# Kernel optimization log

Hardware: AMD Instinct MI355X
Metric: run time of the kernel (lower is better)

Reference implementation:

```python
import jax, jax.numpy as jnp
import numpy as np

DEPTH = 18                      # perfect binary tree depth -> N = 2**DEPTH - 1 nodes
N_NODES = 2 ** DEPTH - 1        # 262143
VOCAB, E, H = 2048, 64, 64


def setup_inputs() -> dict:
    key = jax.random.key(0)
    ks = jax.random.split(key, 10)
    token_ids = jax.random.randint(ks[0], (N_NODES,), 0, VOCAB, dtype=jnp.int32)
    emb = jax.random.normal(ks[1], (VOCAB, E), dtype=jnp.float32)
    emb = emb.at[0].set(0.0)  # padding_idx=0 row is zero in torch
    s = 0.1  # keep gates out of hard saturation
    return {
        "token_ids": token_ids,
        "emb": emb,
        "W_iou": jax.random.normal(ks[2], (3 * H, E), dtype=jnp.float32) * s,
        "b_Wiou": jnp.zeros((3 * H,), dtype=jnp.float32),
        "U_iou": jax.random.normal(ks[3], (3 * H, 2 * H), dtype=jnp.float32) * s,
        "b_Uiou": jnp.zeros((3 * H,), dtype=jnp.float32),
        "W_f": jax.random.normal(ks[4], (2 * H, E), dtype=jnp.float32) * s,
        "b_Wf": jnp.zeros((2 * H,), dtype=jnp.float32),
        "U_f": jax.random.normal(ks[5], (2 * H, 2 * H), dtype=jnp.float32) * s,
        "b_Uf": jnp.zeros((2 * H,), dtype=jnp.float32),
        "depth": DEPTH,
    }


def _tree_lstm(token_ids, emb, W_iou, b_Wiou, U_iou, b_Uiou, W_f, b_Wf, U_f, b_Uf, depth):
    """Level-synchronous bottom-up Binary TreeLSTM over a perfect binary tree.

    Node i has children 2i+1 (left), 2i+2 (right); level l occupies
    indices [2**l - 1, 2**(l+1) - 2]. Children of level-l node k sit at
    offsets 2k, 2k+1 of level l+1, so a reshape gives (left, right) pairs.
    """
    Hd = W_f.shape[0] // 2
    h = c = None
    for l in range(depth - 1, -1, -1):
        start, n = 2 ** l - 1, 2 ** l
        x = emb[token_ids[start:start + n]]                    # [n, E]
        if h is None:  # leaves: zero left/right states (both children zero)
            h_cat = jnp.zeros((n, 2 * Hd), dtype=x.dtype)
            c_lr = jnp.zeros((n, 2, Hd), dtype=x.dtype)
        else:
            h_cat = h.reshape(n, 2 * Hd)                        # [h_l | h_r]
            c_lr = c.reshape(n, 2, Hd)
        iou = jax.nn.sigmoid(x @ W_iou.T + b_Wiou + h_cat @ U_iou.T + b_Uiou)
        i_g, o_g, u_g = jnp.split(iou, 3, axis=1)
        u_g = jnp.tanh(u_g)  # faithful: tanh(sigmoid(u_pre)) as in the source
        f = jax.nn.sigmoid(x @ W_f.T + b_Wf + h_cat @ U_f.T + b_Uf)
        f_l, f_r = f[:, :Hd], f[:, Hd:]
        c = i_g * u_g + f_l * c_lr[:, 0] + f_r * c_lr[:, 1]
        h = o_g * jnp.tanh(c)
    return jnp.stack([h, c])  # [2, 1, H]: root (h, c)


def reference(token_ids, emb, W_iou, b_Wiou, U_iou, b_Uiou, W_f, b_Wf, U_f, b_Uf, depth):
    return _tree_lstm(token_ids, emb, W_iou, b_Wiou, U_iou, b_Uiou,
                      W_f, b_Wf, U_f, b_Uf, depth)
```

## Files before the change

kernel.cpp:

```cpp
#include <hip/hip_runtime.h>

typedef __bf16 bf16;
typedef __bf16 bf16x8 __attribute__((ext_vector_type(8)));
typedef float f32x4 __attribute__((ext_vector_type(4)));

#define DEPTH   18
#define N_NODES ((1 << DEPTH) - 1)
#define KDIM    192
#define RDIM    320
#define A_PAD   200
#define LOG2E   1.4426950408889634f

__device__ __forceinline__ float rcpf(float x) { return __builtin_amdgcn_rcpf(x); }
__device__ __forceinline__ float sig2(float p)  { return rcpf(1.f + exp2f(-p)); }
__device__ __forceinline__ float tanhf_(float x){ return 2.f * rcpf(1.f + exp2f(-2.f * LOG2E * x)) - 1.f; }

__device__ __forceinline__ void gates(const f32x4* acc,
        const float4& bI, const float4& bO, const float4& bU,
        const float4& bL, const float4& bR,
        const float4& cl, const float4& cr, float4& c4, float4& h4) {
    const float* pbI = &bI.x; const float* pbO = &bO.x; const float* pbU = &bU.x;
    const float* pbL = &bL.x; const float* pbR = &bR.x;
    const float* pcl = &cl.x; const float* pcr = &cr.x;
    float* pc4 = &c4.x; float* ph4 = &h4.x;
#pragma unroll
    for (int r = 0; r < 4; r++) {
        float i_g = sig2(acc[0][r] + pbI[r]);
        float o_g = sig2(acc[1][r] + pbO[r]);
        float u_g = tanhf_(sig2(acc[2][r] + pbU[r]));
        float fl  = sig2(acc[3][r] + pbL[r]);
        float fr  = sig2(acc[4][r] + pbR[r]);
        float c = i_g * u_g + fl * pcl[r] + fr * pcr[r];
        pc4[r] = c;
        ph4[r] = o_g * tanhf_(c);
    }
}

__global__ void prep_all(const float* __restrict__ emb,
                     const float* __restrict__ W_iou, const float* __restrict__ U_iou,
                     const float* __restrict__ W_f,   const float* __restrict__ U_f,
                     const float* __restrict__ b_Wiou, const float* __restrict__ b_Uiou,
                     const float* __restrict__ b_Wf,   const float* __restrict__ b_Uf,
                     bf16* __restrict__ Wcat, float* __restrict__ bias, bf16* __restrict__ emb16,
                     bf16* __restrict__ leafH, float* __restrict__ leafC) {
    __shared__ __align__(16) bf16 Wl[192 * 72];
    __shared__ __align__(16) bf16 Al[64 * 72];
    const int blk = blockIdx.x, tid = threadIdx.x;
    if (blk < 512) {
        int t = blk * 256 + tid;
        emb16[t] = (bf16)emb[t];
        if (t < RDIM * KDIM) {
            int r = t / KDIM, k = t % KDIM;
            float v;
            if (r < 192) v = (k < 64) ? W_iou[r * 64 + k] : U_iou[r * 128 + (k - 64)];
            else { int rr = r - 192; v = (k < 64) ? W_f[rr * 64 + k] : U_f[rr * 128 + (k - 64)]; }
            Wcat[t] = (bf16)(v * LOG2E);
        }
        if (t < RDIM)
            bias[t] = ((t < 192) ? (b_Wiou[t] + b_Uiou[t]) : (b_Wf[t - 192] + b_Uf[t - 192])) * LOG2E;
        return;
    }
    const int v0 = (blk - 512) * 64;
    for (int i = tid; i < 192 * 64; i += 256) {
        int r = i >> 6, k = i & 63;
        Wl[r * 72 + k] = (bf16)(W_iou[i] * LOG2E);
    }
    for (int i = tid; i < 64 * 64; i += 256) {
        int r = i >> 6, k = i & 63;
        Al[r * 72 + k] = (bf16)emb[(v0 << 6) + i];
    }
    __syncthreads();
    const int wave = tid >> 6, lane = tid & 63;
    const int l15 = lane & 15, quad = lane >> 4;
    const int jw = (wave & 3) * 16, jb = jw + quad * 4;

    f32x4 acc[4][3];
#pragma unroll
    for (int t = 0; t < 4; t++)
#pragma unroll
        for (int g = 0; g < 3; g++) acc[t][g] = (f32x4){0.f, 0.f, 0.f, 0.f};
#pragma unroll
    for (int kb = 0; kb < 2; kb++) {
        bf16x8 wfrag[3], nfrag[4];
#pragma unroll
        for (int g = 0; g < 3; g++)
            wfrag[g] = *(const bf16x8*)(&Wl[(g * 64 + jw + l15) * 72 + kb * 32 + quad * 8]);
#pragma unroll
        for (int t = 0; t < 4; t++)
            nfrag[t] = *(const bf16x8*)(&Al[(t * 16 + l15) * 72 + kb * 32 + quad * 8]);
#pragma unroll
        for (int t = 0; t < 4; t++)
#pragma unroll
            for (int g = 0; g < 3; g++)
                acc[t][g] = __builtin_amdgcn_mfma_f32_16x16x32_bf16(wfrag[g], nfrag[t], acc[t][g], 0, 0, 0);
    }
    float4 bW, bU_;
    bW = *(const float4*)(b_Wiou + jb);       bU_ = *(const float4*)(b_Uiou + jb);
    float4 bI = make_float4((bW.x + bU_.x) * LOG2E, (bW.y + bU_.y) * LOG2E, (bW.z + bU_.z) * LOG2E, (bW.w + bU_.w) * LOG2E);
    bW = *(const float4*)(b_Wiou + 64 + jb);  bU_ = *(const float4*)(b_Uiou + 64 + jb);
    float4 bO = make_float4((bW.x + bU_.x) * LOG2E, (bW.y + bU_.y) * LOG2E, (bW.z + bU_.z) * LOG2E, (bW.w + bU_.w) * LOG2E);
    bW = *(const float4*)(b_Wiou + 128 + jb); bU_ = *(const float4*)(b_Uiou + 128 + jb);
    float4 bU = make_float4((bW.x + bU_.x) * LOG2E, (bW.y + bU_.y) * LOG2E, (bW.z + bU_.z) * LOG2E, (bW.w + bU_.w) * LOG2E);
    const float* pbI = &bI.x; const float* pbO = &bO.x; const float* pbU = &bU.x;
#pragma unroll
    for (int t = 0; t < 4; t++) {
        int v = v0 + t * 16 + l15;
        float4 c4; float* pc4 = &c4.x;
        union { bf16 h[4]; uint2 u; } hp;
#pragma unroll
        for (int r = 0; r < 4; r++) {
            float i_g = sig2(acc[t][0][r] + pbI[r]);
            float o_g = sig2(acc[t][1][r] + pbO[r]);
            float u_g = tanhf_(sig2(acc[t][2][r] + pbU[r]));
            float c = i_g * u_g;
            pc4[r] = c;
            hp.h[r] = (bf16)(o_g * tanhf_(c));
        }
        *(float4*)(leafC + (size_t)v * 64 + jb) = c4;
        *(uint2*)(leafH + (size_t)v * 64 + jb) = hp.u;
    }
}

__global__ __launch_bounds__(256) void pair_pass(
        const bf16* __restrict__ Wcat, const float* __restrict__ bias,
        const bf16* __restrict__ emb16, const int* __restrict__ token_ids,
        const bf16* __restrict__ leafH, const float* __restrict__ leafC,
        bf16* __restrict__ H, float* __restrict__ c_buf) {
    __shared__ __align__(16) bf16 A1[64 * A_PAD];
    __shared__ __align__(16) bf16 A2[32 * A_PAD];
    float* Cc = (float*)A1;
    const int tid = threadIdx.x;
    const int c0 = blockIdx.x * 64;
    const int p0 = c0 >> 1;
    const int sc = 65535, sp = 32767;

    for (int ch = tid; ch < 64 * 8; ch += 256) {
        int row = ch >> 3, k8 = (ch & 7) << 3;
        int tok = token_ids[sc + c0 + row];
        *(uint4*)&A1[row * A_PAD + k8] = *(const uint4*)(emb16 + tok * 64 + k8);
    }
    for (int ch = tid; ch < 64 * 16; ch += 256) {
        int row = ch >> 4, half = (ch >> 3) & 1, k8 = (ch & 7) << 3;
        int gnc = sc + c0 + row;
        int tok = token_ids[2 * gnc + 1 + half];
        *(uint4*)&A1[row * A_PAD + 64 + half * 64 + k8] = *(const uint4*)(leafH + (size_t)tok * 64 + k8);
    }
    for (int ch = tid; ch < 32 * 8; ch += 256) {
        int row = ch >> 3, k8 = (ch & 7) << 3;
        int tok = token_ids[sp + p0 + row];
        *(uint4*)&A2[row * A_PAD + k8] = *(const uint4*)(emb16 + tok * 64 + k8);
    }
    __syncthreads();

    const int wave = tid >> 6, lane = tid & 63;
    const int l15 = lane & 15, quad = lane >> 4;
    const int jw = wave * 16, jb = jw + quad * 4;

    f32x4 acc[4][5];
#pragma unroll
    for (int t = 0; t < 4; t++)
#pragma unroll
        for (int g = 0; g < 5; g++) acc[t][g] = (f32x4){0.f, 0.f, 0.f, 0.f};
#pragma unroll
    for (int kb = 0; kb < 6; kb++) {
        bf16x8 wfrag[5], nfrag[4];
#pragma unroll
        for (int g = 0; g < 5; g++)
            wfrag[g] = *(const bf16x8*)(Wcat + (g * 64 + jw + l15) * KDIM + kb * 32 + quad * 8);
#pragma unroll
        for (int t = 0; t < 4; t++)
            nfrag[t] = *(const bf16x8*)(&A1[(t * 16 + l15) * A_PAD + kb * 32 + quad * 8]);
#pragma unroll
        for (int t = 0; t < 4; t++)
#pragma unroll
            for (int g = 0; g < 5; g++)
                acc[t][g] = __builtin_amdgcn_mfma_f32_16x16x32_bf16(wfrag[g], nfrag[t], acc[t][g], 0, 0, 0);
    }
    __syncthreads();

    const float4 bI = *(const float4*)(bias + jb);
    const float4 bO = *(const float4*)(bias + 64 + jb);
    const float4 bU = *(const float4*)(bias + 128 + jb);
    const float4 bL = *(const float4*)(bias + 192 + jb);
    const float4 bR = *(const float4*)(bias + 256 + jb);

#pragma unroll
    for (int t = 0; t < 4; t++) {
        const int ci = t * 16 + l15;
        const int gnc = sc + c0 + ci;
        int tkl = token_ids[2 * gnc + 1], tkr = token_ids[2 * gnc + 2];
        float4 cl = *(const float4*)(leafC + (size_t)tkl * 64 + jb);
        float4 cr = *(const float4*)(leafC + (size_t)tkr * 64 + jb);
        float4 c4, h4;
        gates(acc[t], bI, bO, bU, bL, bR, cl, cr, c4, h4);
        union { bf16 h[4]; uint2 u; } hp;
        const float* ph4 = &h4.x;
#pragma unroll
        for (int r = 0; r < 4; r++) hp.h[r] = (bf16)ph4[r];
        *(float4*)(Cc + ci * 68 + jb) = c4;
        *(uint2*)(&A2[(ci >> 1) * A_PAD + 64 + (ci & 1) * 64 + jb]) = hp.u;
    }
    __syncthreads();

    f32x4 pacc[2][5];
#pragma unroll
    for (int t = 0; t < 2; t++)
#pragma unroll
        for (int g = 0; g < 5; g++) pacc[t][g] = (f32x4){0.f, 0.f, 0.f, 0.f};
#pragma unroll
    for (int kb = 0; kb < 6; kb++) {
        bf16x8 wfrag[5], nfrag[2];
#pragma unroll
        for (int g = 0; g < 5; g++)
            wfrag[g] = *(const bf16x8*)(Wcat + (g * 64 + jw + l15) * KDIM + kb * 32 + quad * 8);
#pragma unroll
        for (int t = 0; t < 2; t++)
            nfrag[t] = *(const bf16x8*)(&A2[(t * 16 + l15) * A_PAD + kb * 32 + quad * 8]);
#pragma unroll
        for (int t = 0; t < 2; t++)
#pragma unroll
            for (int g = 0; g < 5; g++)
                pacc[t][g] = __builtin_amdgcn_mfma_f32_16x16x32_bf16(wfrag[g], nfrag[t], pacc[t][g], 0, 0, 0);
    }
#pragma unroll
    for (int t = 0; t < 2; t++) {
        const int p = t * 16 + l15;
        const int gp = sp + p0 + p;
        float4 cl = *(const float4*)(Cc + (2 * p) * 68 + jb);
        float4 cr = *(const float4*)(Cc + (2 * p + 1) * 68 + jb);
        float4 c4, h4;
        gates(pacc[t], bI, bO, bU, bL, bR, cl, cr, c4, h4);
        union { bf16 h[4]; uint2 u; } hp;
        const float* ph4 = &h4.x;
#pragma unroll
        for (int r = 0; r < 4; r++) hp.h[r] = (bf16)ph4[r];
        *(float4*)(c_buf + (size_t)gp * 64 + jb) = c4;
        *(uint2*)(H + (size_t)gp * 64 + jb) = hp.u;
    }
}

__global__ __launch_bounds__(512, 2) void mid_pass(
        const bf16* __restrict__ Wcat, const float* __restrict__ bias,
        const bf16* __restrict__ emb16, const int* __restrict__ token_ids,
        bf16* __restrict__ H, float* __restrict__ c_buf) {
    __shared__ __align__(16) bf16 A0[64 * A_PAD];
    __shared__ __align__(16) bf16 A1[32 * A_PAD];
    const int tid = threadIdx.x, blk = blockIdx.x;
    const int wave = tid >> 6, lane = tid & 63;
    const int l15 = lane & 15, quad = lane >> 4;
    const int wj = wave & 3, wt = wave >> 2;
    const int jw = wj * 16, jb = jw + quad * 4;

    {
        int row = tid >> 3, k8 = (tid & 7) << 3;
        int tok = token_ids[16383 + blk * 64 + row];
        *(uint4*)&A0[row * A_PAD + k8] = *(const uint4*)(emb16 + tok * 64 + k8);
    }
    for (int ch = tid; ch < 1024; ch += 512) {
        int row = ch >> 4, k8 = (ch & 15) << 3;
        int gnc = 16383 + blk * 64 + row;
        *(uint4*)&A0[row * A_PAD + 64 + k8] = *(const uint4*)(H + (size_t)(2 * gnc + 1) * 64 + k8);
    }

    bf16x8 Wf[5][6];
#pragma unroll
    for (int g = 0; g < 5; g++)
#pragma unroll
        for (int kb = 0; kb < 6; kb++)
            Wf[g][kb] = *(const bf16x8*)(Wcat + (g * 64 + jw + l15) * KDIM + kb * 32 + quad * 8);

    const float4 bI = *(const float4*)(bias + jb);
    const float4 bO = *(const float4*)(bias + 64 + jb);
    const float4 bU = *(const float4*)(bias + 128 + jb);
    const float4 bL = *(const float4*)(bias + 192 + jb);
    const float4 bR = *(const float4*)(bias + 256 + jb);
    __syncthreads();

    bf16* Acur = A0;
    bf16* Anx  = A1;
    for (int l = 14; l >= 8; l--) {
        const int m = 1 << (l - 8);
        const int s = (1 << l) - 1, o = blk * m;
        const int T = (m + 15) >> 4;
        for (int ti = wt; ti < T; ti += 2) {
            int idx0 = ti * 16 + l15;
            int idx = idx0 < m ? idx0 : m - 1;
            int gn = s + o + idx;
            float4 cl = *(const float4*)(c_buf + (size_t)(2 * gn + 1) * 64 + jb);
            float4 cr = *(const float4*)(c_buf + (size_t)(2 * gn + 2) * 64 + jb);
            f32x4 acc[5];
#pragma unroll
            for (int g = 0; g < 5; g++) acc[g] = (f32x4){0.f, 0.f, 0.f, 0.f};
#pragma unroll
            for (int kb = 0; kb < 6; kb++) {
                bf16x8 nf = *(const bf16x8*)(&Acur[idx * A_PAD + kb * 32 + quad * 8]);
#pragma unroll
                for (int g = 0; g < 5; g++)
                    acc[g] = __builtin_amdgcn_mfma_f32_16x16x32_bf16(Wf[g][kb], nf, acc[g], 0, 0, 0);
            }
            float4 c4, h4;
            gates(acc, bI, bO, bU, bL, bR, cl, cr, c4, h4);
            if (idx0 < m) {
                union { bf16 h[4]; uint2 u; } hp;
                const float* ph4 = &h4.x;
#pragma unroll
                for (int r = 0; r < 4; r++) hp.h[r] = (bf16)ph4[r];
                *(float4*)(c_buf + (size_t)gn * 64 + jb) = c4;
                if (l > 8)
                    *(uint2*)(&Anx[(idx >> 1) * A_PAD + 64 + (idx & 1) * 64 + jb]) = hp.u;
                else
                    *(uint2*)(H + (size_t)gn * 64 + jb) = hp.u;
            }
        }
        if (l > 8) {
            int mn = m >> 1, sn = (1 << (l - 1)) - 1, on = blk * mn;
            for (int ch = tid; ch < mn * 8; ch += 512) {
                int row = ch >> 3, k8 = (ch & 7) << 3;
                int tok = token_ids[sn + on + row];
                *(uint4*)&Anx[row * A_PAD + k8] = *(const uint4*)(emb16 + tok * 64 + k8);
            }
        }
        __syncthreads();
        bf16* tmp = Acur; Acur = Anx; Anx = tmp;
    }
}

__global__ __launch_bounds__(512) void tail_pass(
        const bf16* __restrict__ Wcat, const float* __restrict__ bias,
        const bf16* __restrict__ emb16, const int* __restrict__ token_ids,
        const bf16* __restrict__ H, const float* __restrict__ c_buf,
        float* __restrict__ out) {
    __shared__ __align__(16) bf16 A[255 * A_PAD];
    __shared__ __align__(16) float C0[128 * 68];
    __shared__ __align__(16) float C1[64 * 68];
    const int tid = threadIdx.x;
    const int wave = tid >> 6, lane = tid & 63;
    const int l15 = lane & 15, quad = lane >> 4;
    const int wj = wave & 3, wt = wave >> 2;
    const int jw = wj * 16, jb = jw + quad * 4;

    float4 cl7[4], cr7[4];
#pragma unroll
    for (int q = 0; q < 4; q++) {
        int idx = (wt + 2 * q) * 16 + l15;
        int gn = 127 + idx;
        cl7[q] = *(const float4*)(c_buf + (size_t)(2 * gn + 1) * 64 + jb);
        cr7[q] = *(const float4*)(c_buf + (size_t)(2 * gn + 2) * 64 + jb);
    }

    for (int ch = tid; ch < 255 * 8; ch += 512) {
        int row = ch >> 3, k8 = (ch & 7) << 3;
        int l = 31 - __clz(255 - row);
        int idx = row - 256 + (2 << l);
        int gn = (1 << l) - 1 + idx;
        int tok = token_ids[gn];
        *(uint4*)&A[row * A_PAD + k8] = *(const uint4*)(emb16 + tok * 64 + k8);
    }
    for (int ch = tid; ch < 128 * 16; ch += 512) {
        int row = ch >> 4, k8 = (ch & 15) << 3;
        *(uint4*)&A[row * A_PAD + 64 + k8] =
            *(const uint4*)(H + (size_t)(255 + 2 * row) * 64 + k8);
    }

    bf16x8 Wf[5][6];
#pragma unroll
    for (int g = 0; g < 5; g++)
#pragma unroll
        for (int kb = 0; kb < 6; kb++)
            Wf[g][kb] = *(const bf16x8*)(Wcat + (g * 64 + jw + l15) * KDIM + kb * 32 + quad * 8);

    const float4 bI = *(const float4*)(bias + jb);
    const float4 bO = *(const float4*)(bias + 64 + jb);
    const float4 bU = *(const float4*)(bias + 128 + jb);
    const float4 bL = *(const float4*)(bias + 192 + jb);
    const float4 bR = *(const float4*)(bias + 256 + jb);
    __syncthreads();

#pragma unroll
    for (int q = 0; q < 4; q++) {
        const int idx = (wt + 2 * q) * 16 + l15;
        f32x4 acc[5];
#pragma unroll
        for (int g = 0; g < 5; g++) acc[g] = (f32x4){0.f, 0.f, 0.f, 0.f};
#pragma unroll
        for (int kb = 0; kb < 6; kb++) {
            bf16x8 nf = *(const bf16x8*)(&A[idx * A_PAD + kb * 32 + quad * 8]);
#pragma unroll
            for (int g = 0; g < 5; g++)
                acc[g] = __builtin_amdgcn_mfma_f32_16x16x32_bf16(Wf[g][kb], nf, acc[g], 0, 0, 0);
        }
        float4 c4, h4;
        gates(acc, bI, bO, bU, bL, bR, cl7[q], cr7[q], c4, h4);
        union { bf16 h[4]; uint2 u; } hp;
        const float* ph4 = &h4.x;
#pragma unroll
        for (int r = 0; r < 4; r++) hp.h[r] = (bf16)ph4[r];
        *(float4*)(C0 + idx * 68 + jb) = c4;
        *(uint2*)(&A[(128 + (idx >> 1)) * A_PAD + 64 + (idx & 1) * 64 + jb]) = hp.u;
    }
    __syncthreads();

    float* Ccur = C0;
    float* Cnx  = C1;
    for (int l = 6; l >= 0; l--) {
        const int n = 1 << l;
        const int off  = 256 - 2 * n;
        const int offn = 256 - n;
        const int T = (n + 15) >> 4;
        for (int ti = wt; ti < T; ti += 2) {
            int idx0 = ti * 16 + l15;
            int idx = idx0 < n ? idx0 : n - 1;
            float4 cl = *(const float4*)(Ccur + (2 * idx) * 68 + jb);
            float4 cr = *(const float4*)(Ccur + (2 * idx + 1) * 68 + jb);
            f32x4 acc[5];
#pragma unroll
            for (int g = 0; g < 5; g++) acc[g] = (f32x4){0.f, 0.f, 0.f, 0.f};
#pragma unroll
            for (int kb = 0; kb < 6; kb++) {
                bf16x8 nf = *(const bf16x8*)(&A[(off + idx) * A_PAD + kb * 32 + quad * 8]);
#pragma unroll
                for (int g = 0; g < 5; g++)
                    acc[g] = __builtin_amdgcn_mfma_f32_16x16x32_bf16(Wf[g][kb], nf, acc[g], 0, 0, 0);
            }
            float4 c4, h4;
            gates(acc, bI, bO, bU, bL, bR, cl, cr, c4, h4);
            if (idx0 < n) {
                if (l > 0) {
                    union { bf16 h[4]; uint2 u; } hp;
                    const float* ph4 = &h4.x;
#pragma unroll
                    for (int r = 0; r < 4; r++) hp.h[r] = (bf16)ph4[r];
                    *(float4*)(Cnx + idx * 68 + jb) = c4;
                    *(uint2*)(&A[(offn + (idx >> 1)) * A_PAD + 64 + (idx & 1) * 64 + jb]) = hp.u;
                } else {
                    *(float4*)(out + jb) = h4;
                    *(float4*)(out + 64 + jb) = c4;
                }
            }
        }
        __syncthreads();
        float* t = Ccur; Ccur = Cnx; Cnx = t;
    }
}

extern "C" void kernel_launch(void* const* d_in, const int* in_sizes, int n_in,
                              void* d_out, int out_size, void* d_ws, size_t ws_size,
                              hipStream_t stream) {
    const int*   token_ids = (const int*)d_in[0];
    const float* emb       = (const float*)d_in[1];
    const float* W_iou     = (const float*)d_in[2];
    const float* b_Wiou    = (const float*)d_in[3];
    const float* U_iou     = (const float*)d_in[4];
    const float* b_Uiou    = (const float*)d_in[5];
    const float* W_f       = (const float*)d_in[6];
    const float* b_Wf      = (const float*)d_in[7];
    const float* U_f       = (const float*)d_in[8];
    const float* b_Uf      = (const float*)d_in[9];
    float* out = (float*)d_out;

    char* ws = (char*)d_ws;
    bf16*  Wcat  = (bf16*)ws;
    float* bias  = (float*)(ws + 122880);
    bf16*  emb16 = (bf16*)(ws + 124160);
    bf16*  leafH = (bf16*)(ws + 386304);
    float* leafC = (float*)(ws + 648448);
    bf16*  H     = (bf16*)(ws + 1172736);
    float* c_buf = (float*)(ws + 34727040);

    prep_all<<<544, 256, 0, stream>>>(emb, W_iou, U_iou, W_f, U_f,
                                      b_Wiou, b_Uiou, b_Wf, b_Uf,
                                      Wcat, bias, emb16, leafH, leafC);
    pair_pass<<<1024, 256, 0, stream>>>(Wcat, bias, emb16, token_ids, leafH, leafC, H, c_buf);
    mid_pass<<<256, 512, 0, stream>>>(Wcat, bias, emb16, token_ids, H, c_buf);
    tail_pass<<<1, 512, 0, stream>>>(Wcat, bias, emb16, token_ids, H, c_buf, out);
}
```

Baseline: 186.5 us.

## Fuse level-16/15 pair pass into mid pass as one persistent kernel

Removes the separate pair_pass launch and folds level 16 into the 256-block mid kernel. Each block now computes 256 level-16 nodes from precomputed leaf states into a larger LDS tile, then continues through levels 15 down to 8 with all data on-chip. This is meant to save one kernel launch and the global H round trip for level 15. In exchange, level 16 runs with fewer, larger blocks, and the LDS footprint (about 150 KB) likely limits residency to one block per CU.

```diff
diff --git a/kernel.cpp b/kernel.cpp
--- a/kernel.cpp
+++ b/kernel.cpp
@@ -121,145 +121,39 @@
     }
 }
 
-__global__ __launch_bounds__(256) void pair_pass(
+__global__ __launch_bounds__(512, 2) void big_pass(
         const bf16* __restrict__ Wcat, const float* __restrict__ bias,
         const bf16* __restrict__ emb16, const int* __restrict__ token_ids,
         const bf16* __restrict__ leafH, const float* __restrict__ leafC,
         bf16* __restrict__ H, float* __restrict__ c_buf) {
-    __shared__ __align__(16) bf16 A1[64 * A_PAD];
-    __shared__ __align__(16) bf16 A2[32 * A_PAD];
-    float* Cc = (float*)A1;
-    const int tid = threadIdx.x;
-    const int c0 = blockIdx.x * 64;
-    const int p0 = c0 >> 1;
-    const int sc = 65535, sp = 32767;
-
-    for (int ch = tid; ch < 64 * 8; ch += 256) {
-        int row = ch >> 3, k8 = (ch & 7) << 3;
-        int tok = token_ids[sc + c0 + row];
-        *(uint4*)&A1[row * A_PAD + k8] = *(const uint4*)(emb16 + tok * 64 + k8);
-    }
-    for (int ch = tid; ch < 64 * 16; ch += 256) {
-        int row = ch >> 4, half = (ch >> 3) & 1, k8 = (ch & 7) << 3;
-        int gnc = sc + c0 + row;
-        int tok = token_ids[2 * gnc + 1 + half];
-        *(uint4*)&A1[row * A_PAD + 64 + half * 64 + k8] = *(const uint4*)(leafH + (size_t)tok * 64 + k8);
-    }
-    for (int ch = tid; ch < 32 * 8; ch += 256) {
-        int row = ch >> 3, k8 = (ch & 7) << 3;
-        int tok = token_ids[sp + p0 + row];
-        *(uint4*)&A2[row * A_PAD + k8] = *(const uint4*)(emb16 + tok * 64 + k8);
-    }
-    __syncthreads();
-
-    const int wave = tid >> 6, lane = tid & 63;
-    const int l15 = lane & 15, quad = lane >> 4;
-    const int jw = wave * 16, jb = jw + quad * 4;
-
-    f32x4 acc[4][5];
-#pragma unroll
-    for (int t = 0; t < 4; t++)
-#pragma unroll
-        for (int g = 0; g < 5; g++) acc[t][g] = (f32x4){0.f, 0.f, 0.f, 0.f};
-#pragma unroll
-    for (int kb = 0; kb < 6; kb++) {
-        bf16x8 wfrag[5], nfrag[4];
-#pragma unroll
-        for (int g = 0; g < 5; g++)
-            wfrag[g] = *(const bf16x8*)(Wcat + (g * 64 + jw + l15) * KDIM + kb * 32 + quad * 8);
-#pragma unroll
-        for (int t = 0; t < 4; t++)
-            nfrag[t] = *(const bf16x8*)(&A1[(t * 16 + l15) * A_PAD + kb * 32 + quad * 8]);
-#pragma unroll
-        for (int t = 0; t < 4; t++)
-#pragma unroll
-            for (int g = 0; g < 5; g++)
-                acc[t][g] = __builtin_amdgcn_mfma_f32_16x16x32_bf16(wfrag[g], nfrag[t], acc[t][g], 0, 0, 0);
-    }
-    __syncthreads();
-
-    const float4 bI = *(const float4*)(bias + jb);
-    const float4 bO = *(const float4*)(bias + 64 + jb);
-    const float4 bU = *(const float4*)(bias + 128 + jb);
-    const float4 bL = *(const float4*)(bias + 192 + jb);
-    const float4 bR = *(const float4*)(bias + 256 + jb);
-
-#pragma unroll
-    for (int t = 0; t < 4; t++) {
-        const int ci = t * 16 + l15;
-        const int gnc = sc + c0 + ci;
-        int tkl = token_ids[2 * gnc + 1], tkr = token_ids[2 * gnc + 2];
-        float4 cl = *(const float4*)(leafC + (size_t)tkl * 64 + jb);
-        float4 cr = *(const float4*)(leafC + (size_t)tkr * 64 + jb);
-        float4 c4, h4;
-        gates(acc[t], bI, bO, bU, bL, bR, cl, cr, c4, h4);
-        union { bf16 h[4]; uint2 u; } hp;
-        const float* ph4 = &h4.x;
-#pragma unroll
-        for (int r = 0; r < 4; r++) hp.h[r] = (bf16)ph4[r];
-        *(float4*)(Cc + ci * 68 + jb) = c4;
-        *(uint2*)(&A2[(ci >> 1) * A_PAD + 64 + (ci & 1) * 64 + jb]) = hp.u;
-    }
-    __syncthreads();
-
-    f32x4 pacc[2][5];
-#pragma unroll
-    for (int t = 0; t < 2; t++)
-#pragma unroll
-        for (int g = 0; g < 5; g++) pacc[t][g] = (f32x4){0.f, 0.f, 0.f, 0.f};
-#pragma unroll
-    for (int kb = 0; kb < 6; kb++) {
-        bf16x8 wfrag[5], nfrag[2];
-#pragma unroll
-        for (int g = 0; g < 5; g++)
-            wfrag[g] = *(const bf16x8*)(Wcat + (g * 64 + jw + l15) * KDIM + kb * 32 + quad * 8);
-#pragma unroll
-        for (int t = 0; t < 2; t++)
-            nfrag[t] = *(const bf16x8*)(&A2[(t * 16 + l15) * A_PAD + kb * 32 + quad * 8]);
-#pragma unroll
-        for (int t = 0; t < 2; t++)
-#pragma unroll
-            for (int g = 0; g < 5; g++)
-                pacc[t][g] = __builtin_amdgcn_mfma_f32_16x16x32_bf16(wfrag[g], nfrag[t], pacc[t][g], 0, 0, 0);
-    }
-#pragma unroll
-    for (int t = 0; t < 2; t++) {
-        const int p = t * 16 + l15;
-        const int gp = sp + p0 + p;
-        float4 cl = *(const float4*)(Cc + (2 * p) * 68 + jb);
-        float4 cr = *(const float4*)(Cc + (2 * p + 1) * 68 + jb);
-        float4 c4, h4;
-        gates(pacc[t], bI, bO, bU, bL, bR, cl, cr, c4, h4);
-        union { bf16 h[4]; uint2 u; } hp;
-        const float* ph4 = &h4.x;
-#pragma unroll
-        for (int r = 0; r < 4; r++) hp.h[r] = (bf16)ph4[r];
-        *(float4*)(c_buf + (size_t)gp * 64 + jb) = c4;
-        *(uint2*)(H + (size_t)gp * 64 + jb) = hp.u;
-    }
-}
-
-__global__ __launch_bounds__(512, 2) void mid_pass(
-        const bf16* __restrict__ Wcat, const float* __restrict__ bias,
-        const bf16* __restrict__ emb16, const int* __restrict__ token_ids,
-        bf16* __restrict__ H, float* __restrict__ c_buf) {
-    __shared__ __align__(16) bf16 A0[64 * A_PAD];
-    __shared__ __align__(16) bf16 A1[32 * A_PAD];
+    __shared__ __align__(16) bf16 A0[256 * A_PAD];
+    __shared__ __align__(16) bf16 A1[128 * A_PAD];
     const int tid = threadIdx.x, blk = blockIdx.x;
     const int wave = tid >> 6, lane = tid & 63;
     const int l15 = lane & 15, quad = lane >> 4;
     const int wj = wave & 3, wt = wave >> 2;
     const int jw = wj * 16, jb = jw + quad * 4;
 
-    {
-        int row = tid >> 3, k8 = (tid & 7) << 3;
-        int tok = token_ids[16383 + blk * 64 + row];
+    const int base16 = 65535 + blk * 256;
+
+    for (int ch = tid; ch < 256 * 8; ch += 512) {
+        int row = ch >> 3, k8 = (ch & 7) << 3;
+        int tok = token_ids[base16 + row];
         *(uint4*)&A0[row * A_PAD + k8] = *(const uint4*)(emb16 + tok * 64 + k8);
     }
-    for (int ch = tid; ch < 1024; ch += 512) {
-        int row = ch >> 4, k8 = (ch & 15) << 3;
-        int gnc = 16383 + blk * 64 + row;
-        *(uint4*)&A0[row * A_PAD + 64 + k8] = *(const uint4*)(H + (size_t)(2 * gnc + 1) * 64 + k8);
+    for (int ch = tid; ch < 256 * 16; ch += 512) {
+        int row = ch >> 4, half = (ch >> 3) & 1, k8 = (ch & 7) << 3;
+        int tok = token_ids[2 * (base16 + row) + 1 + half];
+        *(uint4*)&A0[row * A_PAD + 64 + half * 64 + k8] = *(const uint4*)(leafH + (size_t)tok * 64 + k8);
+    }
+
+    int tkl16[8], tkr16[8];
+#pragma unroll
+    for (int q = 0; q < 8; q++) {
+        int idx = (wt + 2 * q) * 16 + l15;
+        int gn = base16 + idx;
+        tkl16[q] = token_ids[2 * gn + 1];
+        tkr16[q] = token_ids[2 * gn + 2];
     }
 
     bf16x8 Wf[5][6];
@@ -276,9 +170,41 @@
     const float4 bR = *(const float4*)(bias + 256 + jb);
     __syncthreads();
 
-    bf16* Acur = A0;
-    bf16* Anx  = A1;
-    for (int l = 14; l >= 8; l--) {
+#pragma unroll
+    for (int q = 0; q < 8; q++) {
+        const int idx = (wt + 2 * q) * 16 + l15;
+        const int gn = base16 + idx;
+        float4 cl = *(const float4*)(leafC + (size_t)tkl16[q] * 64 + jb);
+        float4 cr = *(const float4*)(leafC + (size_t)tkr16[q] * 64 + jb);
+        f32x4 acc[5];
+#pragma unroll
+        for (int g = 0; g < 5; g++) acc[g] = (f32x4){0.f, 0.f, 0.f, 0.f};
+#pragma unroll
+        for (int kb = 0; kb < 6; kb++) {
+            bf16x8 nf = *(const bf16x8*)(&A0[idx * A_PAD + kb * 32 + quad * 8]);
+#pragma unroll
+            for (int g = 0; g < 5; g++)
+                acc[g] = __builtin_amdgcn_mfma_f32_16x16x32_bf16(Wf[g][kb], nf, acc[g], 0, 0, 0);
+        }
+        float4 c4, h4;
+        gates(acc, bI, bO, bU, bL, bR, cl, cr, c4, h4);
+        union { bf16 h[4]; uint2 u; } hp;
+        const float* ph4 = &h4.x;
+#pragma unroll
+        for (int r = 0; r < 4; r++) hp.h[r] = (bf16)ph4[r];
+        *(float4*)(c_buf + (size_t)gn * 64 + jb) = c4;
+        *(uint2*)(&A1[(idx >> 1) * A_PAD + 64 + (idx & 1) * 64 + jb]) = hp.u;
+    }
+    for (int ch = tid; ch < 128 * 8; ch += 512) {
+        int row = ch >> 3, k8 = (ch & 7) << 3;
+        int tok = token_ids[32767 + blk * 128 + row];
+        *(uint4*)&A1[row * A_PAD + k8] = *(const uint4*)(emb16 + tok * 64 + k8);
+    }
+    __syncthreads();
+
+    bf16* Acur = A1;
+    bf16* Anx  = A0;
+    for (int l = 15; l >= 8; l--) {
         const int m = 1 << (l - 8);
         const int s = (1 << l) - 1, o = blk * m;
         const int T = (m + 15) >> 4;
@@ -470,7 +396,6 @@
     prep_all<<<544, 256, 0, stream>>>(emb, W_iou, U_iou, W_f, U_f,
                                       b_Wiou, b_Uiou, b_Wf, b_Uf,
                                       Wcat, bias, emb16, leafH, leafC);
-    pair_pass<<<1024, 256, 0, stream>>>(Wcat, bias, emb16, token_ids, leafH, leafC, H, c_buf);
-    mid_pass<<<256, 512, 0, stream>>>(Wcat, bias, emb16, token_ids, H, c_buf);
+    big_pass<<<256, 512, 0, stream>>>(Wcat, bias, emb16, token_ids, leafH, leafC, H, c_buf);
     tail_pass<<<1, 512, 0, stream>>>(Wcat, bias, emb16, token_ids, H, c_buf, out);
 }
```

New measurement: 167.3 us. -10.3%, faster.
